# Performance work log

Hardware: AMD Instinct MI355X
Metric: run time of the kernel (lower is better)

Reference implementation:

```python
import jax, jax.numpy as jnp
import numpy as np

BLOCKSIZE = 64  # elements per quantization block


def setup_inputs() -> dict:
    key = jax.random.key(0)
    k1, k2, k3, k4 = jax.random.split(key, 4)
    out_features, in_features = 11008, 4096
    tokens = 8192  # batch 4 * seq 2048
    n = out_features * in_features
    x = jax.random.normal(k1, (tokens, in_features), dtype=jnp.float32)
    codes = jax.random.randint(k2, (n,), 0, 16, dtype=jnp.int32)
    absmax = jax.random.uniform(k3, (n // BLOCKSIZE,), dtype=jnp.float32)
    # NF4-style codebook (16 quantization levels)
    codebook = jnp.array(
        [-1.0, -0.6962, -0.5251, -0.3949, -0.2844, -0.1848, -0.0911, 0.0,
         0.0796, 0.1609, 0.2461, 0.3379, 0.4407, 0.5626, 0.7230, 1.0],
        dtype=jnp.float32)
    bias = jax.random.normal(k4, (out_features,), dtype=jnp.float32)
    return {"x": x, "codes": codes, "absmax": absmax,
            "codebook": codebook, "bias": bias}


def reference(x, codes, absmax, codebook, bias):
    out_features, in_features = 11008, 4096
    # Dequantize: codebook lookup, then per-block scale.  [n] -> [out, in]
    w = codebook[codes].reshape(-1, BLOCKSIZE) * absmax[:, None]
    w = w.reshape(out_features, in_features)
    # y = x @ W.T + b
    y = jnp.einsum('ti,oi->to', x, w) + bias
    return y
```

## Files before the change

### kernel.cpp

```cpp
#include <hip/hip_runtime.h>
#include <hip/hip_bf16.h>
#include <stdint.h>

#define TOKENS 8192
#define OUTF   11008
#define INF    4096
#define NCODES (45088768)

typedef __bf16 bf16x8 __attribute__((ext_vector_type(8)));
typedef float  f32x4  __attribute__((ext_vector_type(4)));

__device__ __forceinline__ unsigned short f32_to_bf16_rne(float f) {
    union { float f; unsigned int u; } v; v.f = f;
    unsigned int u = v.u;
    unsigned int r = u + 0x7fffu + ((u >> 16) & 1u);
    return (unsigned short)(r >> 16);
}

__global__ __launch_bounds__(256) void dequant_w(const int* __restrict__ codes,
                                                 const float* __restrict__ absmax,
                                                 const float* __restrict__ codebook,
                                                 unsigned short* __restrict__ wq) {
    __shared__ float cb[16];
    if (threadIdx.x < 16) cb[threadIdx.x] = codebook[threadIdx.x];
    __syncthreads();
    size_t idx = ((size_t)blockIdx.x * 256 + threadIdx.x) * 8;
    float am = absmax[idx >> 6];
    const int4* cp = (const int4*)(codes + idx);
    int4 c0 = cp[0];
    int4 c1 = cp[1];
    union { unsigned short s[8]; uint4 v; } u;
    u.s[0] = f32_to_bf16_rne(cb[c0.x] * am);
    u.s[1] = f32_to_bf16_rne(cb[c0.y] * am);
    u.s[2] = f32_to_bf16_rne(cb[c0.z] * am);
    u.s[3] = f32_to_bf16_rne(cb[c0.w] * am);
    u.s[4] = f32_to_bf16_rne(cb[c1.x] * am);
    u.s[5] = f32_to_bf16_rne(cb[c1.y] * am);
    u.s[6] = f32_to_bf16_rne(cb[c1.z] * am);
    u.s[7] = f32_to_bf16_rne(cb[c1.w] * am);
    *(uint4*)(wq + idx) = u.v;
}

__global__ __launch_bounds__(256) void cast_x(const float* __restrict__ x,
                                              unsigned short* __restrict__ xq) {
    size_t idx = ((size_t)blockIdx.x * 256 + threadIdx.x) * 8;
    float4 a = *(const float4*)(x + idx);
    float4 b = *(const float4*)(x + idx + 4);
    union { unsigned short s[8]; uint4 v; } u;
    u.s[0] = f32_to_bf16_rne(a.x);
    u.s[1] = f32_to_bf16_rne(a.y);
    u.s[2] = f32_to_bf16_rne(a.z);
    u.s[3] = f32_to_bf16_rne(a.w);
    u.s[4] = f32_to_bf16_rne(b.x);
    u.s[5] = f32_to_bf16_rne(b.y);
    u.s[6] = f32_to_bf16_rne(b.z);
    u.s[7] = f32_to_bf16_rne(b.w);
    *(uint4*)(xq + idx) = u.v;
}

#define BM 256
#define BN 256
#define BK 64

#define GLLDS(SRC, DST)                                                                   \
    __builtin_amdgcn_global_load_lds((const __attribute__((address_space(1))) void*)(SRC),\
                                     (__attribute__((address_space(3))) void*)(DST), 16, 0, 0)

#define STAGE_A(KT, HALF, BUF) do {                                                       \
    const unsigned short* _s = gA + (size_t)(HALF) * (128 * INF) + (size_t)(KT) * BK;     \
    GLLDS(_s,                   &lA[BUF][(HALF) * 8192 + tid * 8]);                       \
    GLLDS(_s + (size_t)64 * INF, &lA[BUF][(HALF) * 8192 + tid * 8 + 4096]); } while (0)

#define STAGE_B(KT, HALF, BUF) do {                                                       \
    const unsigned short* _s = gB + (size_t)(HALF) * (128 * INF) + (size_t)(KT) * BK;     \
    GLLDS(_s,                   &lB[BUF][(HALF) * 8192 + tid * 8]);                       \
    GLLDS(_s + (size_t)64 * INF, &lB[BUF][(HALF) * 8192 + tid * 8 + 4096]); } while (0)

#define READS(AD, BD, BUF, MH, NH) do {                                                   \
    _Pragma("unroll") for (int i = 0; i < 4; ++i) {                                       \
        AD[i][0] = *(const bf16x8*)&lA[BUF][(MH) * 8192 + i * 1024 + aRow + sw0];         \
        AD[i][1] = *(const bf16x8*)&lA[BUF][(MH) * 8192 + i * 1024 + aRow + sw1]; }       \
    _Pragma("unroll") for (int j = 0; j < 2; ++j) {                                       \
        BD[j][0] = *(const bf16x8*)&lB[BUF][(NH) * 8192 + j * 1024 + bRow + sw0];         \
        BD[j][1] = *(const bf16x8*)&lB[BUF][(NH) * 8192 + j * 1024 + bRow + sw1]; } } while (0)

#define MFMA_Q(AS, BS, MH, NH) do {                                                       \
    __builtin_amdgcn_s_setprio(1);                                                        \
    _Pragma("unroll") for (int kc = 0; kc < 2; ++kc)                                      \
    _Pragma("unroll") for (int i = 0; i < 4; ++i)                                         \
    _Pragma("unroll") for (int j = 0; j < 2; ++j)                                         \
        acc[MH][i][NH][j] = __builtin_amdgcn_mfma_f32_16x16x32_bf16(                      \
            AS[i][kc], BS[j][kc], acc[MH][i][NH][j], 0, 0, 0);                            \
    __builtin_amdgcn_s_setprio(0); } while (0)

#define BARRM  do { asm volatile("" ::: "memory"); __builtin_amdgcn_s_barrier();          \
                    asm volatile("" ::: "memory"); } while (0)
#define LGKM0  asm volatile("s_waitcnt lgkmcnt(0)" ::: "memory")
#define VMC(N) asm volatile("s_waitcnt vmcnt(" #N ")" ::: "memory")
#define SCHED0 __builtin_amdgcn_sched_barrier(0)

__global__ __launch_bounds__(512, 2) void gemm_bf16_8p(const unsigned short* __restrict__ Xb,
                                                       const unsigned short* __restrict__ Wb,
                                                       const float* __restrict__ bias,
                                                       float* __restrict__ out) {
    __shared__ __align__(16) unsigned short lA[2][BM * BK];
    __shared__ __align__(16) unsigned short lB[2][BN * BK];

    const int bid  = blockIdx.x;
    const int xcd  = bid & 7;
    const int loc  = bid >> 3;
    const int mt   = xcd * 4 + (loc & 3);
    const int nt   = loc >> 2;
    const int m0   = mt * BM;
    const int n0   = nt * BN;

    const int tid  = threadIdx.x;
    const int lane = tid & 63;
    const int wave = tid >> 6;
    const int wm_l = wave >> 2;
    const int wn_l = wave & 3;

    const int frow = lane & 15;
    const int klan = lane >> 4;
    const int f7   = lane & 7;
    const int sw0  = ((klan)     ^ f7) * 8;
    const int sw1  = ((klan + 4) ^ f7) * 8;
    const int aRow = (wm_l * 64 + frow) * BK;
    const int bRow = (wn_l * 32 + frow) * BK;

    const int rl   = tid >> 3;
    const int gsw  = (tid & 7) ^ (rl & 7);
    const unsigned short* gA = Xb + (size_t)(m0 + rl) * INF + gsw * 8;
    const unsigned short* gB = Wb + (size_t)(n0 + rl) * INF + gsw * 8;

    f32x4 acc[2][4][2][2];
#pragma unroll
    for (int mh = 0; mh < 2; ++mh)
#pragma unroll
        for (int i = 0; i < 4; ++i)
#pragma unroll
            for (int nh = 0; nh < 2; ++nh)
#pragma unroll
                for (int j = 0; j < 2; ++j)
#pragma unroll
                    for (int r = 0; r < 4; ++r) acc[mh][i][nh][j][r] = 0.0f;

    bf16x8 a0[4][2], b0[2][2];
    bf16x8 a1[4][2], b1[2][2];

    STAGE_A(0, 0, 0); STAGE_B(0, 1, 0); STAGE_A(0, 1, 0); STAGE_B(0, 0, 0);
    STAGE_A(1, 0, 1); STAGE_B(1, 1, 1);
    VMC(4);
    BARRM;
    READS(a0, b0, 0, 0, 0);

    for (int it = 0; it < 31; ++it) {
        const int kt1 = 2 * it + 1, kt2 = 2 * it + 2, kt3 = 2 * it + 3;
        BARRM; LGKM0; STAGE_A(kt1, 1, 1); READS(a1, b1, 0, 0, 1); SCHED0; MFMA_Q(a0, b0, 0, 0);
        BARRM; LGKM0; STAGE_B(kt1, 0, 1); READS(a0, b0, 0, 1, 1); SCHED0; MFMA_Q(a1, b1, 0, 1);
        BARRM; LGKM0; STAGE_A(kt2, 0, 0); READS(a1, b1, 0, 1, 0); SCHED0; MFMA_Q(a0, b0, 1, 1);
        BARRM; LGKM0; VMC(2); BARRM;
        STAGE_B(kt2, 1, 0); READS(a0, b0, 1, 0, 0); SCHED0; MFMA_Q(a1, b1, 1, 0);
        BARRM; LGKM0; STAGE_A(kt2, 1, 0); READS(a1, b1, 1, 0, 1); SCHED0; MFMA_Q(a0, b0, 0, 0);
        BARRM; LGKM0; STAGE_B(kt2, 0, 0); READS(a0, b0, 1, 1, 1); SCHED0; MFMA_Q(a1, b1, 0, 1);
        BARRM; LGKM0; STAGE_A(kt3, 0, 1); READS(a1, b1, 1, 1, 0); SCHED0; MFMA_Q(a0, b0, 1, 1);
        BARRM; LGKM0; VMC(2); BARRM;
        STAGE_B(kt3, 1, 1); READS(a0, b0, 0, 0, 0); SCHED0; MFMA_Q(a1, b1, 1, 0);
    }

    BARRM; LGKM0; STAGE_A(63, 1, 1); READS(a1, b1, 0, 0, 1); SCHED0; MFMA_Q(a0, b0, 0, 0);
    BARRM; LGKM0; STAGE_B(63, 0, 1); READS(a0, b0, 0, 1, 1); SCHED0; MFMA_Q(a1, b1, 0, 1);
    BARRM; LGKM0;                    READS(a1, b1, 0, 1, 0); SCHED0; MFMA_Q(a0, b0, 1, 1);
    BARRM; LGKM0; VMC(0); BARRM;     READS(a0, b0, 1, 0, 0); SCHED0; MFMA_Q(a1, b1, 1, 0);
    BARRM; LGKM0;                    READS(a1, b1, 1, 0, 1); SCHED0; MFMA_Q(a0, b0, 0, 0);
    BARRM; LGKM0;                    READS(a0, b0, 1, 1, 1); SCHED0; MFMA_Q(a1, b1, 0, 1);
    BARRM; LGKM0;                    READS(a1, b1, 1, 1, 0); SCHED0; MFMA_Q(a0, b0, 1, 1);
    BARRM; LGKM0;                                            SCHED0; MFMA_Q(a1, b1, 1, 0);

    const int crow = (lane >> 4) * 4;
    const int ccol = lane & 15;
#pragma unroll
    for (int mh = 0; mh < 2; ++mh)
#pragma unroll
        for (int nh = 0; nh < 2; ++nh)
#pragma unroll
            for (int j = 0; j < 2; ++j) {
                const int n = n0 + nh * 128 + wn_l * 32 + j * 16 + ccol;
                const float bv = bias[n];
#pragma unroll
                for (int i = 0; i < 4; ++i) {
                    const int m = m0 + mh * 128 + wm_l * 64 + i * 16 + crow;
#pragma unroll
                    for (int r = 0; r < 4; ++r) {
                        const float v = acc[mh][i][nh][j][r] + bv;
                        __builtin_nontemporal_store(v, &out[(size_t)(m + r) * OUTF + n]);
                    }
                }
            }
}

__global__ __launch_bounds__(256) void fused_fallback(const float* __restrict__ x,
                                                      const int* __restrict__ codes,
                                                      const float* __restrict__ absmax,
                                                      const float* __restrict__ codebook,
                                                      const float* __restrict__ bias,
                                                      float* __restrict__ out) {
    __shared__ float xs[64][17];
    __shared__ float wsm[64][17];
    __shared__ float cb[16];
    const int tid = threadIdx.x;
    if (tid < 16) cb[tid] = codebook[tid];
    const int m0 = blockIdx.y * 64, n0 = blockIdx.x * 64;
    float acc[4][4] = {};
    const int tr = tid >> 4, tc = tid & 15;
    for (int k0 = 0; k0 < INF; k0 += 16) {
        __syncthreads();
#pragma unroll
        for (int i = 0; i < 4; i++) {
            int e = i * 256 + tid;
            int r = e >> 4, c = e & 15;
            xs[r][c] = x[(size_t)(m0 + r) * INF + k0 + c];
            size_t widx = (size_t)(n0 + r) * INF + k0 + c;
            wsm[r][c] = cb[codes[widx]] * absmax[widx >> 6];
        }
        __syncthreads();
#pragma unroll
        for (int kk = 0; kk < 16; kk++) {
            float xv[4], wv[4];
#pragma unroll
            for (int i = 0; i < 4; i++) xv[i] = xs[tr * 4 + i][kk];
#pragma unroll
            for (int j = 0; j < 4; j++) wv[j] = wsm[tc * 4 + j][kk];
#pragma unroll
            for (int i = 0; i < 4; i++)
#pragma unroll
                for (int j = 0; j < 4; j++) acc[i][j] += xv[i] * wv[j];
        }
    }
#pragma unroll
    for (int i = 0; i < 4; i++)
#pragma unroll
        for (int j = 0; j < 4; j++) {
            int m = m0 + tr * 4 + i, n = n0 + tc * 4 + j;
            out[(size_t)m * OUTF + n] = acc[i][j] + bias[n];
        }
}

extern "C" void kernel_launch(void* const* d_in, const int* in_sizes, int n_in,
                              void* d_out, int out_size, void* d_ws, size_t ws_size,
                              hipStream_t stream) {
    const float* x        = (const float*)d_in[0];
    const int*   codes    = (const int*)d_in[1];
    const float* absmax   = (const float*)d_in[2];
    const float* codebook = (const float*)d_in[3];
    const float* bias     = (const float*)d_in[4];
    float* out = (float*)d_out;

    const size_t wbytes = (size_t)NCODES * 2;
    const size_t xbytes = (size_t)TOKENS * INF * 2;

    if (ws_size >= wbytes + xbytes) {
        unsigned short* wq = (unsigned short*)d_ws;
        unsigned short* xq = (unsigned short*)((char*)d_ws + wbytes);
        dequant_w<<<NCODES / 2048, 256, 0, stream>>>(codes, absmax, codebook, wq);
        cast_x<<<(TOKENS * INF) / 2048, 256, 0, stream>>>(x, xq);
        gemm_bf16_8p<<<dim3((TOKENS / BM) * (OUTF / BN)), 512, 0, stream>>>(xq, wq, bias, out);
    } else {
        dim3 grid(OUTF / 64, TOKENS / 64);
        fused_fallback<<<grid, 256, 0, stream>>>(x, codes, absmax, codebook, bias, out);
    }
}
```

Before: 1.423 ms.

## Switch GEMM to 32x32x16 MFMA with single-buffered register fragments and new schedule

Replaces the 16x16x32 bf16 MFMA tiles with 32x32x16 MFMAs, which cuts the number of LDS fragment reads per FLOP and the instruction count. Register double-buffering (a0/a1, b0/b1) is replaced by a single fragment set. The explicit lgkmcnt waits and sched barriers are dropped in favour of plain barriers around each MFMA quarter, and staging runs one half-tile further ahead. The epilogue uses regular stores instead of nontemporal ones. LDS-read latency is now exposed before each MFMA burst because there is no register ping-pong, and removing the explicit sched and wait controls hands ordering back to the compiler.

```diff
diff --git a/kernel.cpp b/kernel.cpp
--- a/kernel.cpp
+++ b/kernel.cpp
@@ -8,7 +8,7 @@
 #define NCODES (45088768)
 
 typedef __bf16 bf16x8 __attribute__((ext_vector_type(8)));
-typedef float  f32x4  __attribute__((ext_vector_type(4)));
+typedef float  f32x16 __attribute__((ext_vector_type(16)));
 
 __device__ __forceinline__ unsigned short f32_to_bf16_rne(float f) {
     union { float f; unsigned int u; } v; v.f = f;
@@ -76,28 +76,25 @@
     GLLDS(_s,                   &lB[BUF][(HALF) * 8192 + tid * 8]);                       \
     GLLDS(_s + (size_t)64 * INF, &lB[BUF][(HALF) * 8192 + tid * 8 + 4096]); } while (0)
 
-#define READS(AD, BD, BUF, MH, NH) do {                                                   \
-    _Pragma("unroll") for (int i = 0; i < 4; ++i) {                                       \
-        AD[i][0] = *(const bf16x8*)&lA[BUF][(MH) * 8192 + i * 1024 + aRow + sw0];         \
-        AD[i][1] = *(const bf16x8*)&lA[BUF][(MH) * 8192 + i * 1024 + aRow + sw1]; }       \
-    _Pragma("unroll") for (int j = 0; j < 2; ++j) {                                       \
-        BD[j][0] = *(const bf16x8*)&lB[BUF][(NH) * 8192 + j * 1024 + bRow + sw0];         \
-        BD[j][1] = *(const bf16x8*)&lB[BUF][(NH) * 8192 + j * 1024 + bRow + sw1]; } } while (0)
-
-#define MFMA_Q(AS, BS, MH, NH) do {                                                       \
+#define LOAD_A32(BUF, MH) do { _Pragma("unroll")                                          \
+    for (int mg = 0; mg < 2; ++mg) { _Pragma("unroll")                                    \
+        for (int ks = 0; ks < 4; ++ks)                                                    \
+            a[mg][ks] = *(const bf16x8*)&lA[BUF][(MH) * 8192 + mg * 2048 + aBase + gk[ks]]; } } while (0)
+
+#define LOAD_B32(BUF, NH) do { _Pragma("unroll")                                          \
+    for (int ks = 0; ks < 4; ++ks)                                                        \
+        b[ks] = *(const bf16x8*)&lB[BUF][(NH) * 8192 + bBase + gk[ks]]; } while (0)
+
+#define MFMA_Q32(MH, NH) do {                                                             \
     __builtin_amdgcn_s_setprio(1);                                                        \
-    _Pragma("unroll") for (int kc = 0; kc < 2; ++kc)                                      \
-    _Pragma("unroll") for (int i = 0; i < 4; ++i)                                         \
-    _Pragma("unroll") for (int j = 0; j < 2; ++j)                                         \
-        acc[MH][i][NH][j] = __builtin_amdgcn_mfma_f32_16x16x32_bf16(                      \
-            AS[i][kc], BS[j][kc], acc[MH][i][NH][j], 0, 0, 0);                            \
+    _Pragma("unroll") for (int ks = 0; ks < 4; ++ks)                                      \
+    _Pragma("unroll") for (int mg = 0; mg < 2; ++mg)                                      \
+        acc[MH][NH][mg] = __builtin_amdgcn_mfma_f32_32x32x16_bf16(                        \
+            a[mg][ks], b[ks], acc[MH][NH][mg], 0, 0, 0);                                  \
     __builtin_amdgcn_s_setprio(0); } while (0)
 
-#define BARRM  do { asm volatile("" ::: "memory"); __builtin_amdgcn_s_barrier();          \
-                    asm volatile("" ::: "memory"); } while (0)
-#define LGKM0  asm volatile("s_waitcnt lgkmcnt(0)" ::: "memory")
+#define BARR   __builtin_amdgcn_s_barrier()
 #define VMC(N) asm volatile("s_waitcnt vmcnt(" #N ")" ::: "memory")
-#define SCHED0 __builtin_amdgcn_sched_barrier(0)
 
 __global__ __launch_bounds__(512, 2) void gemm_bf16_8p(const unsigned short* __restrict__ Xb,
                                                        const unsigned short* __restrict__ Wb,
@@ -120,83 +117,90 @@
     const int wm_l = wave >> 2;
     const int wn_l = wave & 3;
 
-    const int frow = lane & 15;
-    const int klan = lane >> 4;
-    const int f7   = lane & 7;
-    const int sw0  = ((klan)     ^ f7) * 8;
-    const int sw1  = ((klan + 4) ^ f7) * 8;
-    const int aRow = (wm_l * 64 + frow) * BK;
-    const int bRow = (wn_l * 32 + frow) * BK;
+    const int l31 = lane & 31;
+    const int lh  = lane >> 5;
+    const int f7  = lane & 7;
+    int gk[4];
+#pragma unroll
+    for (int ks = 0; ks < 4; ++ks) gk[ks] = ((ks * 2 + lh) ^ f7) * 8;
+    const int aBase = (wm_l * 64 + l31) * BK;
+    const int bBase = (wn_l * 32 + l31) * BK;
 
     const int rl   = tid >> 3;
     const int gsw  = (tid & 7) ^ (rl & 7);
     const unsigned short* gA = Xb + (size_t)(m0 + rl) * INF + gsw * 8;
     const unsigned short* gB = Wb + (size_t)(n0 + rl) * INF + gsw * 8;
 
-    f32x4 acc[2][4][2][2];
+    f32x16 acc[2][2][2];
 #pragma unroll
     for (int mh = 0; mh < 2; ++mh)
 #pragma unroll
-        for (int i = 0; i < 4; ++i)
-#pragma unroll
-            for (int nh = 0; nh < 2; ++nh)
-#pragma unroll
-                for (int j = 0; j < 2; ++j)
-#pragma unroll
-                    for (int r = 0; r < 4; ++r) acc[mh][i][nh][j][r] = 0.0f;
-
-    bf16x8 a0[4][2], b0[2][2];
-    bf16x8 a1[4][2], b1[2][2];
+        for (int nh = 0; nh < 2; ++nh)
+#pragma unroll
+            for (int mg = 0; mg < 2; ++mg)
+#pragma unroll
+                for (int r = 0; r < 16; ++r) acc[mh][nh][mg][r] = 0.0f;
+
+    bf16x8 a[2][4], b[4];
 
     STAGE_A(0, 0, 0); STAGE_B(0, 1, 0); STAGE_A(0, 1, 0); STAGE_B(0, 0, 0);
-    STAGE_A(1, 0, 1); STAGE_B(1, 1, 1);
-    VMC(4);
-    BARRM;
-    READS(a0, b0, 0, 0, 0);
+    STAGE_A(1, 0, 1); STAGE_B(1, 1, 1); STAGE_A(1, 1, 1);
+    VMC(6);
+    BARR;
 
     for (int it = 0; it < 31; ++it) {
         const int kt1 = 2 * it + 1, kt2 = 2 * it + 2, kt3 = 2 * it + 3;
-        BARRM; LGKM0; STAGE_A(kt1, 1, 1); READS(a1, b1, 0, 0, 1); SCHED0; MFMA_Q(a0, b0, 0, 0);
-        BARRM; LGKM0; STAGE_B(kt1, 0, 1); READS(a0, b0, 0, 1, 1); SCHED0; MFMA_Q(a1, b1, 0, 1);
-        BARRM; LGKM0; STAGE_A(kt2, 0, 0); READS(a1, b1, 0, 1, 0); SCHED0; MFMA_Q(a0, b0, 1, 1);
-        BARRM; LGKM0; VMC(2); BARRM;
-        STAGE_B(kt2, 1, 0); READS(a0, b0, 1, 0, 0); SCHED0; MFMA_Q(a1, b1, 1, 0);
-        BARRM; LGKM0; STAGE_A(kt2, 1, 0); READS(a1, b1, 1, 0, 1); SCHED0; MFMA_Q(a0, b0, 0, 0);
-        BARRM; LGKM0; STAGE_B(kt2, 0, 0); READS(a0, b0, 1, 1, 1); SCHED0; MFMA_Q(a1, b1, 0, 1);
-        BARRM; LGKM0; STAGE_A(kt3, 0, 1); READS(a1, b1, 1, 1, 0); SCHED0; MFMA_Q(a0, b0, 1, 1);
-        BARRM; LGKM0; VMC(2); BARRM;
-        STAGE_B(kt3, 1, 1); READS(a0, b0, 0, 0, 0); SCHED0; MFMA_Q(a1, b1, 1, 0);
+        LOAD_A32(0, 0); LOAD_B32(0, 0); STAGE_B(kt1, 0, 1);
+        BARR; MFMA_Q32(0, 0); BARR;
+        LOAD_B32(0, 1); STAGE_A(kt2, 0, 0);
+        BARR; MFMA_Q32(0, 1); BARR;
+        LOAD_A32(0, 1); STAGE_B(kt2, 1, 0);
+        BARR; MFMA_Q32(1, 1); BARR;
+        LOAD_B32(0, 0); STAGE_A(kt2, 1, 0);
+        BARR; MFMA_Q32(1, 0); VMC(6); BARR;
+        LOAD_A32(1, 0); LOAD_B32(1, 0); STAGE_B(kt2, 0, 0);
+        BARR; MFMA_Q32(0, 0); BARR;
+        LOAD_B32(1, 1); STAGE_A(kt3, 0, 1);
+        BARR; MFMA_Q32(0, 1); BARR;
+        LOAD_A32(1, 1); STAGE_B(kt3, 1, 1);
+        BARR; MFMA_Q32(1, 1); BARR;
+        LOAD_B32(1, 0); STAGE_A(kt3, 1, 1);
+        BARR; MFMA_Q32(1, 0); VMC(6); BARR;
     }
 
-    BARRM; LGKM0; STAGE_A(63, 1, 1); READS(a1, b1, 0, 0, 1); SCHED0; MFMA_Q(a0, b0, 0, 0);
-    BARRM; LGKM0; STAGE_B(63, 0, 1); READS(a0, b0, 0, 1, 1); SCHED0; MFMA_Q(a1, b1, 0, 1);
-    BARRM; LGKM0;                    READS(a1, b1, 0, 1, 0); SCHED0; MFMA_Q(a0, b0, 1, 1);
-    BARRM; LGKM0; VMC(0); BARRM;     READS(a0, b0, 1, 0, 0); SCHED0; MFMA_Q(a1, b1, 1, 0);
-    BARRM; LGKM0;                    READS(a1, b1, 1, 0, 1); SCHED0; MFMA_Q(a0, b0, 0, 0);
-    BARRM; LGKM0;                    READS(a0, b0, 1, 1, 1); SCHED0; MFMA_Q(a1, b1, 0, 1);
-    BARRM; LGKM0;                    READS(a1, b1, 1, 1, 0); SCHED0; MFMA_Q(a0, b0, 1, 1);
-    BARRM; LGKM0;                                            SCHED0; MFMA_Q(a1, b1, 1, 0);
-
-    const int crow = (lane >> 4) * 4;
-    const int ccol = lane & 15;
+    LOAD_A32(0, 0); LOAD_B32(0, 0); STAGE_B(63, 0, 1);
+    BARR; MFMA_Q32(0, 0); BARR;
+    LOAD_B32(0, 1);
+    BARR; MFMA_Q32(0, 1); BARR;
+    LOAD_A32(0, 1);
+    BARR; MFMA_Q32(1, 1); BARR;
+    LOAD_B32(0, 0);
+    BARR; MFMA_Q32(1, 0); VMC(0); BARR;
+    LOAD_A32(1, 0); LOAD_B32(1, 0);
+    BARR; MFMA_Q32(0, 0); BARR;
+    LOAD_B32(1, 1);
+    BARR; MFMA_Q32(0, 1); BARR;
+    LOAD_A32(1, 1);
+    BARR; MFMA_Q32(1, 1); BARR;
+    LOAD_B32(1, 0);
+    BARR; MFMA_Q32(1, 0);
+
 #pragma unroll
     for (int mh = 0; mh < 2; ++mh)
 #pragma unroll
-        for (int nh = 0; nh < 2; ++nh)
-#pragma unroll
-            for (int j = 0; j < 2; ++j) {
-                const int n = n0 + nh * 128 + wn_l * 32 + j * 16 + ccol;
-                const float bv = bias[n];
-#pragma unroll
-                for (int i = 0; i < 4; ++i) {
-                    const int m = m0 + mh * 128 + wm_l * 64 + i * 16 + crow;
-#pragma unroll
-                    for (int r = 0; r < 4; ++r) {
-                        const float v = acc[mh][i][nh][j][r] + bv;
-                        __builtin_nontemporal_store(v, &out[(size_t)(m + r) * OUTF + n]);
-                    }
+        for (int nh = 0; nh < 2; ++nh) {
+            const int n = n0 + nh * 128 + wn_l * 32 + l31;
+            const float bv = bias[n];
+#pragma unroll
+            for (int mg = 0; mg < 2; ++mg) {
+                const int mb = m0 + mh * 128 + wm_l * 64 + mg * 32 + 4 * lh;
+#pragma unroll
+                for (int r = 0; r < 16; ++r) {
+                    const int m = mb + (r & 3) + 8 * (r >> 2);
+                    out[(size_t)m * OUTF + n] = acc[mh][nh][mg][r] + bv;
                 }
             }
+        }
 }
 
 __global__ __launch_bounds__(256) void fused_fallback(const float* __restrict__ x,
```

After: 1.305 ms. -8.3%, faster.
